# Kernel optimization log

Measured on AMD Instinct MI355X. Metric: run time of the kernel, lower is better.

## Reference

```python
import jax, jax.numpy as jnp
import numpy as np

B, S, L = 4, 1024, 512          # batch, max_seqlen, actual per-seq length
H, D = 12, 64                   # heads, head_dim
DIM = H * D                     # 768
NNZ = B * L                     # 2048 unpadded tokens


def setup_inputs() -> dict:
    key = jax.random.key(0)
    k1, k2, k3 = jax.random.split(key, 3)
    hidden_states = jax.random.normal(k1, (NNZ, DIM), jnp.float32)
    Wqkv_w = jax.random.normal(k2, (3 * DIM, DIM), jnp.float32) * 0.02
    Wqkv_b = jnp.zeros((3 * DIM,), jnp.float32)
    # ALiBi-style bias; in the real model it also encodes the padding mask (-inf),
    # here random values suffice for a correctness baseline.
    bias = jax.random.normal(k3, (B, H, S, S), jnp.float32) * 0.1
    # each sequence occupies the first L slots of its row in the padded layout
    indices = (jnp.arange(B)[:, None] * S + jnp.arange(L)[None, :]).reshape(-1).astype(jnp.int32)
    cu_seqlens = (jnp.arange(B + 1) * L).astype(jnp.int32)
    attn_mask = jnp.zeros((B, S), jnp.int32).at[:, :L].set(1)
    return dict(hidden_states=hidden_states, Wqkv_w=Wqkv_w, Wqkv_b=Wqkv_b,
                bias=bias, indices=indices, attn_mask=attn_mask,
                cu_seqlens=cu_seqlens, max_seqlen_in_batch=S)


def reference(hidden_states, Wqkv_w, Wqkv_b, bias, indices, attn_mask,
              cu_seqlens, max_seqlen_in_batch):
    b = attn_mask.shape[0]
    s = max_seqlen_in_batch
    # QKV projection on unpadded tokens: (nnz, 3*dim)
    qkv = hidden_states @ Wqkv_w.T + Wqkv_b
    # pad_input: scatter unpadded rows into (b*s) padded layout
    padded = jnp.zeros((b * s, qkv.shape[-1]), qkv.dtype).at[indices].set(qkv)
    qkv = padded.reshape(b, s, 3, H, D)
    q, k, v = qkv[:, :, 0], qkv[:, :, 1], qkv[:, :, 2]  # (b, s, h, d)
    scale = 1.0 / float(np.sqrt(D))
    scores = jnp.einsum('bqhd,bkhd->bhqk', q, k) * scale + bias  # (b,h,s,s)
    probs = jax.nn.softmax(scores, axis=-1)
    ctx = jnp.einsum('bhqk,bkhd->bqhd', probs, v)  # (b, s, h, d)
    # unpad_input_only: gather back rows where attn_mask == 1 (== indices)
    return ctx.reshape(b * s, H * D)[indices]
```

## Files before the change

### kernel.cpp

```cpp
#include <hip/hip_runtime.h>
#include <hip/hip_bf16.h>
#include <cstdint>

typedef short  s16x8 __attribute__((ext_vector_type(8)));
typedef ushort u16x8 __attribute__((ext_vector_type(8)));
typedef ushort u16x4 __attribute__((ext_vector_type(4)));
typedef float  f32x4 __attribute__((ext_vector_type(4)));

#define B_    4
#define S_    1024
#define H_    12
#define D_    64
#define DIM_  768
#define QSCALE 0.18033688011112042f
#define LOG2E  1.4426950408889634f

#define NTAIL 384

#define GLOAD16(gp, lp) \
  __builtin_amdgcn_global_load_lds((const __attribute__((address_space(1))) unsigned int*)(gp), \
                                   (__attribute__((address_space(3))) unsigned int*)(lp), 16, 0, 0)

__device__ __forceinline__ ushort f2bf(float f) {
    __bf16 h = (__bf16)f;
    return __builtin_bit_cast(ushort, h);
}

__device__ __forceinline__ u16x8 cvt8(f32x4 x, f32x4 y) {
    u16x8 r;
    r[0]=f2bf(x[0]); r[1]=f2bf(x[1]); r[2]=f2bf(x[2]); r[3]=f2bf(x[3]);
    r[4]=f2bf(y[0]); r[5]=f2bf(y[1]); r[6]=f2bf(y[2]); r[7]=f2bf(y[3]);
    return r;
}

__global__ __launch_bounds__(256) void prep(
    const float* __restrict__ hidden, const float* __restrict__ W,
    const float* __restrict__ bias, const int* __restrict__ cu,
    ushort* __restrict__ Ah, ushort* __restrict__ Wh, float* __restrict__ T,
    int nh, int nw, int ncvt, int nrows, int nnz)
{
    const int t = threadIdx.x;
    if ((int)blockIdx.x < ncvt) {
        const int total = (nh + nw) >> 3;
        for (int i = blockIdx.x * 256 + t; i < total; i += ncvt * 256) {
            const float* src; ushort* dst; int off = i << 3;
            if (off < nh) { src = hidden; dst = Ah; }
            else          { src = W;      dst = Wh; off -= nh; }
            f32x4 x0 = *(const f32x4*)(src + off);
            f32x4 x1 = *(const f32x4*)(src + off + 4);
            *(u16x8*)(dst + off) = cvt8(x0, x1);
        }
    } else {
        const int blk = blockIdx.x - ncvt;
        const int w = t >> 6, l = t & 63, grp = l >> 4, lc = l & 15;
        for (int rid = blk*16 + w*4 + grp; rid < nrows; rid += NTAIL*16) {
            const int h = rid / nnz;
            const int u = rid - h * nnz;
            int b = 0;
            while (cu[b+1] <= u) b++;
            const int q  = u - cu[b];
            const int Lb = cu[b+1] - cu[b];
            const float* rp = bias + ((size_t)(b*H_ + h)*S_ + q)*S_;
            float s = 0.0f;
            for (int k = Lb + lc*4; k < S_; k += 64) {
                f32x4 v = *(const f32x4*)(rp + k);
                s += exp2f(v[0]*LOG2E) + exp2f(v[1]*LOG2E)
                   + exp2f(v[2]*LOG2E) + exp2f(v[3]*LOG2E);
            }
            s += __shfl_xor(s, 1, 64);
            s += __shfl_xor(s, 2, 64);
            s += __shfl_xor(s, 4, 64);
            s += __shfl_xor(s, 8, 64);
            if (lc == 0) T[(size_t)(b*H_ + h)*S_ + q] = s;
        }
    }
}

__global__ __launch_bounds__(256) void qkv_gemm(
    const ushort* __restrict__ Ah, const ushort* __restrict__ Wh,
    const float* __restrict__ bvec, const int* __restrict__ cu,
    ushort* __restrict__ Qu, ushort* __restrict__ Ku, ushort* __restrict__ Vt)
{
    __shared__ ushort As[128][64];
    __shared__ ushort Bs[128][64];

    const int t  = threadIdx.x;
    const int n0 = blockIdx.x * 128;
    const int m0 = blockIdx.y * 128;
    const int w  = t >> 6, l = t & 63, lg = l >> 4, lc = l & 15;
    const int wm = w >> 1, wn = w & 1;

    const int lrow  = l >> 3;
    const int gslot = (l & 7) ^ lrow;
    const ushort* aS[4]; const ushort* bS[4];
    ushort* aD[4]; ushort* bD[4];
    #pragma unroll
    for (int i = 0; i < 4; i++) {
        const int r = w*32 + i*8;
        aS[i] = Ah + (size_t)(m0 + r + lrow)*DIM_ + gslot*8;
        bS[i] = Wh + (size_t)(n0 + r + lrow)*DIM_ + gslot*8;
        aD[i] = &As[r][0];
        bD[i] = &Bs[r][0];
    }

    f32x4 acc[4][4];
    #pragma unroll
    for (int i = 0; i < 4; i++)
        #pragma unroll
        for (int j = 0; j < 4; j++) acc[i][j] = (f32x4)0.0f;

    for (int k0 = 0; k0 < DIM_; k0 += 64) {
        #pragma unroll
        for (int i = 0; i < 4; i++) {
            GLOAD16(aS[i] + k0, aD[i]);
            GLOAD16(bS[i] + k0, bD[i]);
        }
        __syncthreads();
        s16x8 af[2][4], bf[2][4];
        #pragma unroll
        for (int kk = 0; kk < 2; kk++) {
            #pragma unroll
            for (int mi = 0; mi < 4; mi++) {
                const int r = wm*64 + mi*16 + lc;
                af[kk][mi] = *(const s16x8*)&As[r][(((kk<<2)+lg) ^ (r&7))*8];
            }
            #pragma unroll
            for (int ni = 0; ni < 4; ni++) {
                const int r = wn*64 + ni*16 + lc;
                bf[kk][ni] = *(const s16x8*)&Bs[r][(((kk<<2)+lg) ^ (r&7))*8];
            }
        }
        #pragma unroll
        for (int mi = 0; mi < 4; mi++)
            #pragma unroll
            for (int ni = 0; ni < 4; ni++) {
                acc[mi][ni] = __builtin_amdgcn_mfma_f32_16x16x32_bf16(
                                  af[0][mi], bf[0][ni], acc[mi][ni], 0, 0, 0);
                acc[mi][ni] = __builtin_amdgcn_mfma_f32_16x16x32_bf16(
                                  af[1][mi], bf[1][ni], acc[mi][ni], 0, 0, 0);
            }
        __syncthreads();
    }

    const int sec = n0 / DIM_;
    float bv[4];
    #pragma unroll
    for (int ni = 0; ni < 4; ni++) bv[ni] = bvec[n0 + wn*64 + ni*16 + lc];

    #pragma unroll
    for (int mi = 0; mi < 4; mi++) {
        const int r = m0 + wm*64 + mi*16 + lg*4;
        if (sec == 2) {
            int b = 0;
            while (cu[b+1] <= r) b++;
            const int q = r - cu[b];
            #pragma unroll
            for (int ni = 0; ni < 4; ni++) {
                const int nl = wn*64 + ni*16 + lc + (n0 - 2*DIM_);
                const int h = nl >> 6, d = nl & 63;
                u16x4 pk;
                #pragma unroll
                for (int j = 0; j < 4; j++) pk[j] = f2bf(acc[mi][ni][j] + bv[ni]);
                *(u16x4*)&Vt[((size_t)((b*H_ + h)*64 + d))*S_ + q] = pk;
            }
        } else {
            #pragma unroll
            for (int j = 0; j < 4; j++) {
                #pragma unroll
                for (int ni = 0; ni < 4; ni++) {
                    const int nl = wn*64 + ni*16 + lc + (n0 - sec*DIM_);
                    float v = acc[mi][ni][j] + bv[ni];
                    if (sec == 0) Qu[(size_t)(r+j)*DIM_ + nl] = f2bf(v * QSCALE);
                    else          Ku[(size_t)(r+j)*DIM_ + nl] = f2bf(v);
                }
            }
        }
    }
}

__global__ __launch_bounds__(256) void attn_kernel(
    const ushort* __restrict__ Qu, const ushort* __restrict__ Ku,
    const ushort* __restrict__ Vt, const float* __restrict__ bias,
    const float* __restrict__ T, const int* __restrict__ cu,
    float* __restrict__ out)
{
    const int b  = blockIdx.x >> 4, qt = blockIdx.x & 15;
    const int h  = blockIdx.y;
    const int cu0 = cu[b];
    const int Lb  = cu[b+1] - cu0;
    const int qbase = qt * 64;
    if (qbase >= Lb) return;

    const int t = threadIdx.x, w = t >> 6, l = t & 63, lg = l >> 4, lc = l & 15;

    __shared__ ushort Ks[64][72];
    __shared__ ushort Vs[80][72];
    __shared__ ushort Ps[4][16][72];

    for (int i = t; i < 16*9; i += 256) {
        const int row = 64 + i/9, ch = i%9;
        u16x8 v = (u16x8)0;
        if (row == 64 && ch < 8)
            #pragma unroll
            for (int e = 0; e < 8; e++) v[e] = 0x3F80;
        *(u16x8*)&Vs[row][ch*8] = v;
    }

    const float*  bias_b = bias + (size_t)(b*H_ + h)*S_*S_;
    const ushort* kbase  = Ku + (size_t)cu0*DIM_ + h*64;
    const ushort* vbase  = Vt + (size_t)((b*H_ + h)*64)*S_;

    const int krow = t >> 3, kch = t & 7;

    const int rl = w*16 + lg*4;
    int p_[4]; bool val_[4];
    const float* bpr[4];
    #pragma unroll
    for (int j = 0; j < 4; j++) {
        const int r = qbase + rl + j;
        val_[j] = (r < Lb);
        p_[j]   = val_[j] ? r : (Lb - 1);
        bpr[j]  = bias_b + (size_t)p_[j]*S_;
    }

    int qar = qbase + w*16 + lc; if (qar >= Lb) qar = Lb - 1;
    const ushort* qp = Qu + (size_t)(cu0 + qar)*DIM_ + h*64;
    s16x8 qa0 = *(const s16x8*)(qp + lg*8);
    s16x8 qa1 = *(const s16x8*)(qp + 32 + lg*8);

    f32x4 O[4], lsum;
    #pragma unroll
    for (int d = 0; d < 4; d++) O[d] = (f32x4)0.0f;
    lsum = (f32x4)0.0f;

    float pf[4][4];
    u16x8 kr[2], vr[2];
    #pragma unroll
    for (int f = 0; f < 4; f++)
        #pragma unroll
        for (int j = 0; j < 4; j++) pf[f][j] = bpr[j][f*16 + lc];
    #pragma unroll
    for (int i = 0; i < 2; i++) {
        const int r = krow + i*32;
        const int rc = (r < Lb) ? r : Lb - 1;
        kr[i] = *(const u16x8*)(kbase + (size_t)rc*DIM_ + kch*8);
        vr[i] = *(const u16x8*)(vbase + (size_t)r*S_ + kch*8);
    }

    for (int k0 = 0; k0 < Lb; k0 += 64) {
        __syncthreads();
        #pragma unroll
        for (int i = 0; i < 2; i++) {
            const int r = krow + i*32;
            u16x8 kz = (k0 + r < Lb) ? kr[i] : (u16x8)0;
            *(u16x8*)&Ks[r][kch*8] = kz;
            *(u16x8*)&Vs[r][kch*8] = vr[i];
        }
        __syncthreads();

        f32x4 sc[4];
        #pragma unroll
        for (int f = 0; f < 4; f++)
            #pragma unroll
            for (int j = 0; j < 4; j++) sc[f][j] = pf[f][j] * LOG2E;

        const int kn = k0 + 64;
        if (kn < Lb) {
            #pragma unroll
            for (int f = 0; f < 4; f++)
                #pragma unroll
                for (int j = 0; j < 4; j++) pf[f][j] = bpr[j][kn + f*16 + lc];
            #pragma unroll
            for (int i = 0; i < 2; i++) {
                const int r = krow + i*32;
                const int rc = (kn + r < Lb) ? kn + r : Lb - 1;
                kr[i] = *(const u16x8*)(kbase + (size_t)rc*DIM_ + kch*8);
                vr[i] = *(const u16x8*)(vbase + (size_t)r*S_ + kn + kch*8);
            }
        }

        #pragma unroll
        for (int f = 0; f < 4; f++) {
            s16x8 kb0 = *(const s16x8*)&Ks[f*16 + lc][lg*8];
            s16x8 kb1 = *(const s16x8*)&Ks[f*16 + lc][32 + lg*8];
            sc[f] = __builtin_amdgcn_mfma_f32_16x16x32_bf16(qa0, kb0, sc[f], 0,0,0);
            sc[f] = __builtin_amdgcn_mfma_f32_16x16x32_bf16(qa1, kb1, sc[f], 0,0,0);
        }
        if (k0 + 64 > Lb) {
            #pragma unroll
            for (int f = 0; f < 4; f++) {
                const int kcol = k0 + f*16 + lc;
                if (kcol >= Lb)
                    #pragma unroll
                    for (int j = 0; j < 4; j++) sc[f][j] = -1e30f;
            }
        }

        #pragma unroll
        for (int f = 0; f < 4; f++)
            #pragma unroll
            for (int j = 0; j < 4; j++)
                Ps[w][lg*4 + j][f*16 + lc] = f2bf(exp2f(sc[f][j]));

        s16x8 pa0 = *(const s16x8*)&Ps[w][lc][lg*8];
        s16x8 pa1 = *(const s16x8*)&Ps[w][lc][32 + lg*8];
        #pragma unroll
        for (int df = 0; df < 4; df++) {
            s16x8 vb0 = *(const s16x8*)&Vs[df*16 + lc][lg*8];
            s16x8 vb1 = *(const s16x8*)&Vs[df*16 + lc][32 + lg*8];
            O[df] = __builtin_amdgcn_mfma_f32_16x16x32_bf16(pa0, vb0, O[df], 0,0,0);
            O[df] = __builtin_amdgcn_mfma_f32_16x16x32_bf16(pa1, vb1, O[df], 0,0,0);
        }
        {
            s16x8 ob0 = *(const s16x8*)&Vs[64 + lc][lg*8];
            s16x8 ob1 = *(const s16x8*)&Vs[64 + lc][32 + lg*8];
            lsum = __builtin_amdgcn_mfma_f32_16x16x32_bf16(pa0, ob0, lsum, 0,0,0);
            lsum = __builtin_amdgcn_mfma_f32_16x16x32_bf16(pa1, ob1, lsum, 0,0,0);
        }
    }

    #pragma unroll
    for (int j = 0; j < 4; j++) {
        float lj = lsum[j] + T[(size_t)(b*H_ + h)*S_ + p_[j]];
        float inv = 1.0f / lj;
        inv = __shfl(inv, l & 48, 64);
        if (val_[j]) {
            float* op = out + (size_t)(cu0 + qbase + rl + j)*DIM_ + h*64;
            #pragma unroll
            for (int df = 0; df < 4; df++) op[df*16 + lc] = O[df][j] * inv;
        }
    }
}

extern "C" void kernel_launch(void* const* d_in, const int* in_sizes, int n_in,
                              void* d_out, int out_size, void* d_ws, size_t ws_size,
                              hipStream_t stream)
{
    const float* hidden  = (const float*)d_in[0];
    const float* W       = (const float*)d_in[1];
    const float* bvec    = (const float*)d_in[2];
    const float* bias    = (const float*)d_in[3];
    const int*   cu      = (const int*)d_in[6];
    float*       out     = (float*)d_out;

    const int NNZ = in_sizes[0] / DIM_;
    const int nh  = NNZ * DIM_;
    const int nw  = 3 * DIM_ * DIM_;
    const int ncvt  = (nh + nw) / 8 / 256;
    const int nrows = NNZ * H_;

    char* ws = (char*)d_ws;
    const size_t uB  = (size_t)NNZ * DIM_ * 2;
    const size_t vtB = (size_t)B_ * H_ * 64 * S_ * 2;
    ushort* Qu = (ushort*)(ws);
    ushort* Ku = (ushort*)(ws + uB);
    ushort* Vt = (ushort*)(ws + 2*uB);
    ushort* Ah = (ushort*)(ws + 2*uB + vtB);
    ushort* Wh = (ushort*)(ws + 2*uB + vtB + (size_t)nh*2);
    float*  T  = (float*)(ws + 2*uB + vtB + (size_t)(nh + nw)*2);

    prep<<<ncvt + NTAIL, 256, 0, stream>>>(hidden, W, bias, cu, Ah, Wh, T,
                                           nh, nw, ncvt, nrows, NNZ);

    dim3 gg(3*DIM_/128, NNZ/128);
    qkv_gemm<<<gg, 256, 0, stream>>>(Ah, Wh, bvec, cu, Qu, Ku, Vt);

    dim3 ga(B_*(S_/64), H_);
    attn_kernel<<<ga, 256, 0, stream>>>(Qu, Ku, Vt, bias, T, cu, out);
}
```

Baseline: 64.19 us.

## Fuse fp32-to-bf16 conversion into QKV GEMM and merge with tail-sum kernel

The separate conversion pass that wrote bf16 copies of hidden states and weights is removed. The GEMM now loads fp32 tiles directly, converts them in registers and stores them to padded LDS with a K-step of 32. The GEMM blocks and the bias tail-sum blocks run in one launch, which drops a kernel launch and the intermediate bf16 round trip through memory. In exchange the GEMM loses the async global-to-LDS loads and the swizzled layout, does twice as many K iterations with two barriers each, and re-reads and re-converts fp32 data once per tile.

```diff
diff --git a/kernel.cpp b/kernel.cpp
--- a/kernel.cpp
+++ b/kernel.cpp
@@ -17,10 +17,6 @@
 
 #define NTAIL 384
 
-#define GLOAD16(gp, lp) \
-  __builtin_amdgcn_global_load_lds((const __attribute__((address_space(1))) unsigned int*)(gp), \
-                                   (__attribute__((address_space(3))) unsigned int*)(lp), 16, 0, 0)
-
 __device__ __forceinline__ ushort f2bf(float f) {
     __bf16 h = (__bf16)f;
     return __builtin_bit_cast(ushort, h);
@@ -33,25 +29,17 @@
     return r;
 }
 
-__global__ __launch_bounds__(256) void prep(
+__global__ __launch_bounds__(256) void gemm_tail(
     const float* __restrict__ hidden, const float* __restrict__ W,
-    const float* __restrict__ bias, const int* __restrict__ cu,
-    ushort* __restrict__ Ah, ushort* __restrict__ Wh, float* __restrict__ T,
-    int nh, int nw, int ncvt, int nrows, int nnz)
+    const float* __restrict__ bvec, const float* __restrict__ bias,
+    const int* __restrict__ cu,
+    ushort* __restrict__ Qu, ushort* __restrict__ Ku, ushort* __restrict__ Vt,
+    float* __restrict__ T, int ngemm, int nrows, int nnz)
 {
     const int t = threadIdx.x;
-    if ((int)blockIdx.x < ncvt) {
-        const int total = (nh + nw) >> 3;
-        for (int i = blockIdx.x * 256 + t; i < total; i += ncvt * 256) {
-            const float* src; ushort* dst; int off = i << 3;
-            if (off < nh) { src = hidden; dst = Ah; }
-            else          { src = W;      dst = Wh; off -= nh; }
-            f32x4 x0 = *(const f32x4*)(src + off);
-            f32x4 x1 = *(const f32x4*)(src + off + 4);
-            *(u16x8*)(dst + off) = cvt8(x0, x1);
-        }
-    } else {
-        const int blk = blockIdx.x - ncvt;
+
+    if ((int)blockIdx.x >= ngemm) {
+        const int blk = blockIdx.x - ngemm;
         const int w = t >> 6, l = t & 63, grp = l >> 4, lc = l & 15;
         for (int rid = blk*16 + w*4 + grp; rid < nrows; rid += NTAIL*16) {
             const int h = rid / nnz;
@@ -73,35 +61,20 @@
             s += __shfl_xor(s, 8, 64);
             if (lc == 0) T[(size_t)(b*H_ + h)*S_ + q] = s;
         }
-    }
-}
-
-__global__ __launch_bounds__(256) void qkv_gemm(
-    const ushort* __restrict__ Ah, const ushort* __restrict__ Wh,
-    const float* __restrict__ bvec, const int* __restrict__ cu,
-    ushort* __restrict__ Qu, ushort* __restrict__ Ku, ushort* __restrict__ Vt)
-{
-    __shared__ ushort As[128][64];
-    __shared__ ushort Bs[128][64];
-
-    const int t  = threadIdx.x;
-    const int n0 = blockIdx.x * 128;
-    const int m0 = blockIdx.y * 128;
+        return;
+    }
+
+    __shared__ ushort As[128][40];
+    __shared__ ushort Bs[128][40];
+
+    const int n0 = (blockIdx.x % 18) * 128;
+    const int m0 = (blockIdx.x / 18) * 128;
     const int w  = t >> 6, l = t & 63, lg = l >> 4, lc = l & 15;
     const int wm = w >> 1, wn = w & 1;
 
-    const int lrow  = l >> 3;
-    const int gslot = (l & 7) ^ lrow;
-    const ushort* aS[4]; const ushort* bS[4];
-    ushort* aD[4]; ushort* bD[4];
-    #pragma unroll
-    for (int i = 0; i < 4; i++) {
-        const int r = w*32 + i*8;
-        aS[i] = Ah + (size_t)(m0 + r + lrow)*DIM_ + gslot*8;
-        bS[i] = Wh + (size_t)(n0 + r + lrow)*DIM_ + gslot*8;
-        aD[i] = &As[r][0];
-        bD[i] = &Bs[r][0];
-    }
+    const int srow = t >> 1, shalf = t & 1;
+    const float* aSrc = hidden + (size_t)(m0 + srow) * DIM_ + shalf * 16;
+    const float* bSrc = W      + (size_t)(n0 + srow) * DIM_ + shalf * 16;
 
     f32x4 acc[4][4];
     #pragma unroll
@@ -109,37 +82,32 @@
         #pragma unroll
         for (int j = 0; j < 4; j++) acc[i][j] = (f32x4)0.0f;
 
-    for (int k0 = 0; k0 < DIM_; k0 += 64) {
-        #pragma unroll
-        for (int i = 0; i < 4; i++) {
-            GLOAD16(aS[i] + k0, aD[i]);
-            GLOAD16(bS[i] + k0, bD[i]);
-        }
+    for (int k0 = 0; k0 < DIM_; k0 += 32) {
         __syncthreads();
-        s16x8 af[2][4], bf[2][4];
-        #pragma unroll
-        for (int kk = 0; kk < 2; kk++) {
-            #pragma unroll
-            for (int mi = 0; mi < 4; mi++) {
-                const int r = wm*64 + mi*16 + lc;
-                af[kk][mi] = *(const s16x8*)&As[r][(((kk<<2)+lg) ^ (r&7))*8];
-            }
-            #pragma unroll
-            for (int ni = 0; ni < 4; ni++) {
-                const int r = wn*64 + ni*16 + lc;
-                bf[kk][ni] = *(const s16x8*)&Bs[r][(((kk<<2)+lg) ^ (r&7))*8];
-            }
-        }
+        {
+            const f32x4* a4 = (const f32x4*)(aSrc + k0);
+            f32x4 x0 = a4[0], x1 = a4[1], x2 = a4[2], x3 = a4[3];
+            const f32x4* b4 = (const f32x4*)(bSrc + k0);
+            f32x4 y0 = b4[0], y1 = b4[1], y2 = b4[2], y3 = b4[3];
+            *(u16x8*)&As[srow][shalf*16]     = cvt8(x0, x1);
+            *(u16x8*)&As[srow][shalf*16 + 8] = cvt8(x2, x3);
+            *(u16x8*)&Bs[srow][shalf*16]     = cvt8(y0, y1);
+            *(u16x8*)&Bs[srow][shalf*16 + 8] = cvt8(y2, y3);
+        }
+        __syncthreads();
+        s16x8 af[4], bfr[4];
         #pragma unroll
         for (int mi = 0; mi < 4; mi++)
-            #pragma unroll
-            for (int ni = 0; ni < 4; ni++) {
+            af[mi] = *(const s16x8*)&As[wm*64 + mi*16 + lc][lg*8];
+        #pragma unroll
+        for (int ni = 0; ni < 4; ni++)
+            bfr[ni] = *(const s16x8*)&Bs[wn*64 + ni*16 + lc][lg*8];
+        #pragma unroll
+        for (int mi = 0; mi < 4; mi++)
+            #pragma unroll
+            for (int ni = 0; ni < 4; ni++)
                 acc[mi][ni] = __builtin_amdgcn_mfma_f32_16x16x32_bf16(
-                                  af[0][mi], bf[0][ni], acc[mi][ni], 0, 0, 0);
-                acc[mi][ni] = __builtin_amdgcn_mfma_f32_16x16x32_bf16(
-                                  af[1][mi], bf[1][ni], acc[mi][ni], 0, 0, 0);
-            }
-        __syncthreads();
+                                  af[mi], bfr[ni], acc[mi][ni], 0, 0, 0);
     }
 
     const int sec = n0 / DIM_;
@@ -343,10 +311,8 @@
     const int*   cu      = (const int*)d_in[6];
     float*       out     = (float*)d_out;
 
-    const int NNZ = in_sizes[0] / DIM_;
-    const int nh  = NNZ * DIM_;
-    const int nw  = 3 * DIM_ * DIM_;
-    const int ncvt  = (nh + nw) / 8 / 256;
+    const int NNZ   = in_sizes[0] / DIM_;
+    const int ngemm = 18 * (NNZ / 128);
     const int nrows = NNZ * H_;
 
     char* ws = (char*)d_ws;
@@ -355,15 +321,10 @@
     ushort* Qu = (ushort*)(ws);
     ushort* Ku = (ushort*)(ws + uB);
     ushort* Vt = (ushort*)(ws + 2*uB);
-    ushort* Ah = (ushort*)(ws + 2*uB + vtB);
-    ushort* Wh = (ushort*)(ws + 2*uB + vtB + (size_t)nh*2);
-    float*  T  = (float*)(ws + 2*uB + vtB + (size_t)(nh + nw)*2);
-
-    prep<<<ncvt + NTAIL, 256, 0, stream>>>(hidden, W, bias, cu, Ah, Wh, T,
-                                           nh, nw, ncvt, nrows, NNZ);
-
-    dim3 gg(3*DIM_/128, NNZ/128);
-    qkv_gemm<<<gg, 256, 0, stream>>>(Ah, Wh, bvec, cu, Qu, Ku, Vt);
+    float*  T  = (float*)(ws + 2*uB + vtB);
+
+    gemm_tail<<<ngemm + NTAIL, 256, 0, stream>>>(hidden, W, bvec, bias, cu,
+                                                 Qu, Ku, Vt, T, ngemm, nrows, NNZ);
 
     dim3 ga(B_*(S_/64), H_);
     attn_kernel<<<ga, 256, 0, stream>>>(Qu, Ku, Vt, bias, T, cu, out);
```

Result: faster. 62.33 us (-2.9%).
